# Kernel tuning notes

Measured on AMD Instinct MI355X. Metric: run time of the kernel, lower is better.

Reference implementation:

```python
import jax, jax.numpy as jnp
import numpy as np

STRIDES = [8, 16, 32, 64, 128]
FEAT_SIZES = [(100, 100), (50, 50), (25, 25), (13, 13), (7, 7)]
IMG_H, IMG_W = 800, 800
NUM_CLASSES = 8  # required by the repeat(8) in _loss_single_scale
BATCH, NUM_GT = 8, 50


def _make_anchor_levels():
    """RetinaNet anchors: octave_base_scale=4, scales_per_octave=3, ratios [0.5,1,2]."""
    ratios = np.array([0.5, 1.0, 2.0], dtype=np.float64)
    scales = 4.0 * 2.0 ** (np.arange(3) / 3.0)
    levels = []
    for stride, (fh, fw) in zip(STRIDES, FEAT_SIZES):
        h_r = np.sqrt(ratios)
        w_r = 1.0 / h_r
        ws = (w_r[:, None] * scales[None, :]).reshape(-1) * stride  # [9]
        hs = (h_r[:, None] * scales[None, :]).reshape(-1) * stride
        base = np.stack([-ws / 2, -hs / 2, ws / 2, hs / 2], axis=1)  # [9,4]
        xs = np.arange(fw) * stride
        ys = np.arange(fh) * stride
        xx, yy = np.meshgrid(xs, ys)  # [fh,fw]
        shifts = np.stack([xx, yy, xx, yy], axis=-1).reshape(-1, 4)  # [fh*fw,4]
        anchors = (shifts[:, None, :] + base[None, :, :]).reshape(-1, 4)  # loc-major, A inner
        levels.append(anchors.astype(np.float32))
    return levels


def _pairwise_iou(a, b):
    # a: [K,4], b: [G,4] -> [K,G]
    area_a = (a[:, 2] - a[:, 0]) * (a[:, 3] - a[:, 1])
    area_b = (b[:, 2] - b[:, 0]) * (b[:, 3] - b[:, 1])
    lt = jnp.maximum(a[:, None, :2], b[None, :, :2])
    rb = jnp.minimum(a[:, None, 2:], b[None, :, 2:])
    wh = jnp.clip(rb - lt, 0.0)
    inter = wh[..., 0] * wh[..., 1]
    return inter / (area_a[:, None] + area_b[None, :] - inter)


def _encode(anchors, gts):
    # DeltaXYWH encode, means=0, stds=1
    aw = anchors[:, 2] - anchors[:, 0]
    ah = anchors[:, 3] - anchors[:, 1]
    ax = anchors[:, 0] + 0.5 * aw
    ay = anchors[:, 1] + 0.5 * ah
    gw = gts[:, 2] - gts[:, 0]
    gh = gts[:, 3] - gts[:, 1]
    gx = gts[:, 0] + 0.5 * gw
    gy = gts[:, 1] + 0.5 * gh
    return jnp.stack([(gx - ax) / aw, (gy - ay) / ah,
                      jnp.log(gw / aw), jnp.log(gh / ah)], axis=1)


def _targets_per_image(anchors, tgt_boxes, tgt_cls):
    # MaxIoUMatcher(thresholds=[0.4,0.5], labels=[0,-1,1], low_quality=True)
    inside = ((anchors[:, 0] >= 0) & (anchors[:, 1] >= 0)
              & (anchors[:, 2] <= IMG_W) & (anchors[:, 3] <= IMG_H))
    iou = _pairwise_iou(anchors, tgt_boxes)             # [K,G]
    iou = jnp.where(inside[:, None], iou, -1.0)          # exclude outside anchors
    max_iou = iou.max(axis=1)
    argmax_gt = iou.argmax(axis=1)
    label = jnp.where(max_iou >= 0.5, 1, jnp.where(max_iou >= 0.4, -1, 0))
    gt_max = iou.max(axis=0)                             # [G]
    is_lq = (iou == gt_max[None, :]) & (gt_max[None, :] > 0)
    any_lq = is_lq.any(axis=1)
    G = tgt_boxes.shape[0]
    lq_gt = jnp.where(is_lq, jnp.arange(G)[None, :], -1).max(axis=1)
    matched_gt = jnp.where(any_lq, lq_gt, argmax_gt)
    label = jnp.where(any_lq, 1, label)
    pos = (label == 1) & inside
    neg = (label == 0) & inside
    deltas = _encode(anchors, tgt_boxes[matched_gt])     # [K,4]
    bbox_targets = jnp.where(pos[:, None], deltas, 0.0)
    bbox_weights = jnp.where(pos[:, None], 1.0, 0.0) * jnp.ones((1, 4), jnp.float32)
    labels_out = jnp.where(pos, tgt_cls[matched_gt].astype(jnp.float32), 0.0)
    label_weights = (pos | neg).astype(jnp.float32)
    return labels_out, label_weights, bbox_targets, bbox_weights, pos.sum(), neg.sum()


def _bce_logits(x, t):
    return jnp.maximum(x, 0.0) - x * t + jnp.log1p(jnp.exp(-jnp.abs(x)))


def _loss_level(cls_out, reg_out, labels, lw, bt, bw, num_samples):
    labels = labels.reshape(-1)
    lw = lw.reshape(-1)
    C = NUM_CLASSES
    cls_score = cls_out.transpose(0, 2, 3, 1).reshape(labels.shape[0], C)  # [N*H*W*A, C]
    tgt = jax.nn.one_hot(labels.astype(jnp.int32), C + 1, dtype=jnp.float32)[:, :C]
    lw2 = jnp.tile(lw, 8).reshape(-1, C)  # faithful to label_weights.repeat(8).reshape(-1, C)
    loss_cls = (_bce_logits(cls_score, tgt) * lw2).sum() / num_samples
    bt = bt.reshape(-1, 4)
    bw = bw.reshape(-1, 4)
    pred = reg_out.transpose(0, 2, 3, 1).reshape(-1, 4)
    loss_bbox = (jnp.abs(pred - bt) * bw).sum() / num_samples
    return loss_cls, loss_bbox


def setup_inputs() -> dict:
    key = jax.random.key(0)
    ks = jax.random.split(key, 16)
    inp = {}
    for i, (fh, fw) in enumerate(FEAT_SIZES):
        inp[f"cls{i}"] = jax.random.normal(ks[i], (BATCH, 9 * NUM_CLASSES, fh, fw), jnp.float32)
        inp[f"reg{i}"] = jax.random.normal(ks[5 + i], (BATCH, 9 * 4, fh, fw), jnp.float32)
    xy = jax.random.uniform(ks[10], (BATCH, NUM_GT, 2), minval=0.0, maxval=600.0)
    wh = jax.random.uniform(ks[11], (BATCH, NUM_GT, 2), minval=20.0, maxval=180.0)
    inp["target_boxes"] = jnp.concatenate([xy, xy + wh], axis=-1).astype(jnp.float32)
    inp["target_class_ids"] = jax.random.randint(ks[12], (BATCH, NUM_GT), 0, NUM_CLASSES, jnp.int64 if jax.config.jax_enable_x64 else jnp.int32)
    return inp


def reference(cls0, cls1, cls2, cls3, cls4, reg0, reg1, reg2, reg3, reg4,
              target_boxes, target_class_ids):
    anchor_levels = _make_anchor_levels()
    anchors = jnp.asarray(np.concatenate(anchor_levels, axis=0))  # [K,4]
    num_lvl = [a.shape[0] for a in anchor_levels]
    labels, lw, bt, bw, npos, nneg = jax.vmap(
        lambda b, c: _targets_per_image(anchors, b, c))(target_boxes, target_class_ids)
    num_samples = (npos.sum() + nneg.sum()).astype(jnp.float32)
    offs = np.cumsum([0] + num_lvl)
    cls_outs = [cls0, cls1, cls2, cls3, cls4]
    reg_outs = [reg0, reg1, reg2, reg3, reg4]
    loss_cls_all = jnp.float32(0.0)
    loss_bbox_all = jnp.float32(0.0)
    for i in range(len(num_lvl)):
        s, e = int(offs[i]), int(offs[i + 1])
        lc, lb = _loss_level(cls_outs[i], reg_outs[i], labels[:, s:e], lw[:, s:e],
                             bt[:, s:e], bw[:, s:e], num_samples)
        loss_cls_all = loss_cls_all + lc
        loss_bbox_all = loss_bbox_all + lb
    return loss_cls_all, loss_bbox_all
```

## Files before the change

kernel.cpp:

```cpp
#include <hip/hip_runtime.h>
#include <cstdint>

#define DEVINL __device__ __forceinline__

constexpr int NB = 8;
constexpr int NG = 50;
constexpr int KTOT = 120087;
constexpr int BK = NB * KTOT;

constexpr int L_W[5]   = {100, 50, 25, 13, 7};
constexpr int L_K[5]   = {90000, 22500, 5625, 1521, 441};
constexpr int L_OFF[5] = {0, 90000, 112500, 118125, 119646};
constexpr int L_STR[5] = {8, 16, 32, 64, 128};
constexpr int L_WSB[5] = {0, 720000, 900000, 945000, 957168};

constexpr double HR_T[3] = {0.7071067811865476, 1.0, 1.4142135623730951};
constexpr double WR_T[3] = {1.0 / HR_T[0], 1.0, 1.0 / HR_T[2]};
constexpr double SC_T[3] = {4.0, 5.039684199579493, 6.3496042078727974};

__device__ float4 g_anc[KTOT];
__device__ double g_accs[256][2];
__device__ unsigned g_ns;
__device__ unsigned g_gtmax[NB * NG];
__device__ int8_t g_lab[BK];
__device__ __align__(8) int8_t g_lw[BK];
__device__ int8_t g_pos[BK];
__device__ int8_t g_mg[BK];

DEVINL unsigned encf(float f) {
  unsigned u = __float_as_uint(f);
  return (u & 0x80000000u) ? ~u : (u | 0x80000000u);
}

DEVINL int lvl_of(int k) {
  return (k < 90000) ? 0 : (k < 112500) ? 1 : (k < 118125) ? 2 : (k < 119646) ? 3 : 4;
}

DEVINL float iou_one(float ax0, float ay0, float ax1, float ay1, float areaA,
                     float bx0, float by0, float bx1, float by1, float areaB) {
  float ltx = fmaxf(ax0, bx0);
  float lty = fmaxf(ay0, by0);
  float rbx = fminf(ax1, bx1);
  float rby = fminf(ay1, by1);
  float wx = fmaxf(rbx - ltx, 0.0f);
  float wy = fmaxf(rby - lty, 0.0f);
  float inter = wx * wy;
  return __fdividef(inter, areaA + areaB - inter);
}

__global__ __launch_bounds__(256) void k_setup() {
  if (blockIdx.x == 0) {
    int t = threadIdx.x;
    g_accs[t][0] = 0.0;
    g_accs[t][1] = 0.0;
    if (t == 0) g_ns = 0u;
  }
  int k = blockIdx.x * 256 + threadIdx.x;
  if (k >= KTOT) return;
  int l = lvl_of(k);
  int r = k - L_OFF[l];
  int loc = r / 9;
  int a = r - loc * 9;
  int W = L_W[l];
  int y = loc / W;
  int x = loc - y * W;
  int st = L_STR[l];
  int ridx = a / 3;
  int sidx = a - ridx * 3;
  double wsz = WR_T[ridx] * SC_T[sidx] * (double)st;
  double hsz = HR_T[ridx] * SC_T[sidx] * (double)st;
  double cx = (double)(x * st);
  double cy = (double)(y * st);
  g_anc[k] = make_float4((float)(cx - wsz * 0.5), (float)(cy - hsz * 0.5),
                         (float)(cx + wsz * 0.5), (float)(cy + hsz * 0.5));
}

DEVINL int axis_cand(int xi, int i0, int lo, int hi, int Wm1) {
  int c;
  if (xi < 4) c = i0 - 1 + xi;
  else if (xi == 4) c = lo;
  else if (xi == 5) c = lo + 1;
  else if (xi == 6) c = hi - 1;
  else if (xi == 7) c = hi;
  else if (xi == 8) c = 0;
  else c = Wm1;
  return min(max(c, 0), Wm1);
}

__global__ __launch_bounds__(256) void k_gtmax2(const float* __restrict__ tb) {
  const int bg = blockIdx.x;
  float4 v = reinterpret_cast<const float4*>(tb)[bg];
  const float bx0 = v.x, by0 = v.y, bx1 = v.z, by1 = v.w;
  const float areaB = (bx1 - bx0) * (by1 - by0);
  const float bcx = 0.5f * (bx0 + bx1), bcy = 0.5f * (by0 + by1);

  float m = -1.0f;
  for (int t = threadIdx.x; t < 4500; t += 256) {
    int l = t / 900;
    int rem = t - l * 900;
    int a = rem / 100;
    int rem2 = rem - a * 100;
    int xi = rem2 / 10;
    int yi = rem2 - xi * 10;
    int W = (l == 0) ? 100 : (l == 1) ? 50 : (l == 2) ? 25 : (l == 3) ? 13 : 7;
    int loff = (l == 0) ? 0 : (l == 1) ? 90000 : (l == 2) ? 112500
               : (l == 3) ? 118125 : 119646;
    float stf = (float)(8 << l);
    float4 A0 = g_anc[loff + a];
    float whalf = -A0.x;
    float hhalf = -A0.y;
    int i0x = (int)floorf(bcx / stf);
    int lox = (int)ceilf(whalf / stf);
    int hix = (int)floorf((800.0f - whalf) / stf);
    int i0y = (int)floorf(bcy / stf);
    int loy = (int)ceilf(hhalf / stf);
    int hiy = (int)floorf((800.0f - hhalf) / stf);
    int cx = axis_cand(xi, i0x, lox, hix, W - 1);
    int cy = axis_cand(yi, i0y, loy, hiy, W - 1);
    int k = loff + (cy * W + cx) * 9 + a;
    float4 A = g_anc[k];
    bool inside = (A.x >= 0.0f) & (A.y >= 0.0f) & (A.z <= 800.0f) & (A.w <= 800.0f);
    float areaA = (A.z - A.x) * (A.w - A.y);
    float iou = inside ? iou_one(A.x, A.y, A.z, A.w, areaA,
                                 bx0, by0, bx1, by1, areaB)
                       : -1.0f;
    m = fmaxf(m, iou);
  }
#pragma unroll
  for (int off = 32; off; off >>= 1) m = fmaxf(m, __shfl_down(m, off));
  __shared__ float s_m[4];
  int lane = threadIdx.x & 63, wid = threadIdx.x >> 6;
  if (lane == 0) s_m[wid] = m;
  __syncthreads();
  if (threadIdx.x == 0) {
    float r = fmaxf(fmaxf(s_m[0], s_m[1]), fmaxf(s_m[2], s_m[3]));
    g_gtmax[bg] = encf(r);
  }
}

constexpr int APB = 4;
__global__ __launch_bounds__(256) void k_assign(const float* __restrict__ tb,
                                                const int* __restrict__ tcls) {
  const int b = blockIdx.y;
  __shared__ float s_b[NG][8];
  __shared__ int s_cls[NG];
  __shared__ unsigned s_cnt;
  int tid = threadIdx.x;
  if (tid == 0) s_cnt = 0u;
  if (tid < NG) {
    float4 v = reinterpret_cast<const float4*>(tb)[b * NG + tid];
    s_b[tid][0] = v.x; s_b[tid][1] = v.y; s_b[tid][2] = v.z; s_b[tid][3] = v.w;
    s_b[tid][4] = (v.z - v.x) * (v.w - v.y);
    unsigned gm = g_gtmax[b * NG + tid];
    s_b[tid][5] = (gm > 0x80000000u) ? __uint_as_float(gm ^ 0x80000000u)
                                     : __uint_as_float(0x7FC00000u);
    s_cls[tid] = tcls[b * NG + tid];
  }
  __syncthreads();

  const int base = blockIdx.x * (256 * APB) + tid;
  float Ax0[APB], Ay0[APB], Ax1[APB], Ay1[APB], areaA[APB];
  bool inside[APB];
  float best[APB];
  int arg[APB], lqg[APB];
#pragma unroll
  for (int ap = 0; ap < APB; ++ap) {
    int k = base + ap * 256;
    bool valid = k < KTOT;
    float4 A = g_anc[valid ? k : 0];
    Ax0[ap] = A.x; Ay0[ap] = A.y; Ax1[ap] = A.z; Ay1[ap] = A.w;
    inside[ap] = valid & (A.x >= 0.0f) & (A.y >= 0.0f) & (A.z <= 800.0f) & (A.w <= 800.0f);
    areaA[ap] = (A.z - A.x) * (A.w - A.y);
    best[ap] = -2.0f; arg[ap] = 0; lqg[ap] = -1;
  }

#pragma unroll 5
  for (int g = 0; g < NG; ++g) {
    float gx0 = s_b[g][0], gy0 = s_b[g][1], gx1 = s_b[g][2], gy1 = s_b[g][3];
    float gar = s_b[g][4], qmx = s_b[g][5];
#pragma unroll
    for (int ap = 0; ap < APB; ++ap) {
      float iou = inside[ap] ? iou_one(Ax0[ap], Ay0[ap], Ax1[ap], Ay1[ap], areaA[ap],
                                       gx0, gy0, gx1, gy1, gar)
                             : -1.0f;
      if (iou > best[ap]) { best[ap] = iou; arg[ap] = g; }
      if (iou == qmx) lqg[ap] = g;
    }
  }

  int cnt = 0;
#pragma unroll
  for (int ap = 0; ap < APB; ++ap) {
    int k = base + ap * 256;
    if (k < KTOT) {
      int lab = (best[ap] >= 0.5f) ? 1 : ((best[ap] >= 0.4f) ? -1 : 0);
      int mg = arg[ap];
      if (lqg[ap] >= 0) { lab = 1; mg = lqg[ap]; }
      bool pos = (lab == 1) && inside[ap];
      bool neg = (lab == 0) && inside[ap];
      int l = lvl_of(k);
      int r = k - L_OFF[l];
      int widx = L_WSB[l] + b * L_K[l] + r;
      g_lab[widx] = pos ? (int8_t)s_cls[mg] : (int8_t)0;
      g_lw[widx] = (pos || neg) ? 1 : 0;
      g_pos[widx] = pos ? 1 : 0;
      g_mg[widx] = (int8_t)mg;
      cnt += (pos || neg) ? 1 : 0;
    }
  }
#pragma unroll
  for (int off = 32; off; off >>= 1) cnt += __shfl_down(cnt, off);
  if ((tid & 63) == 0 && cnt) atomicAdd(&s_cnt, (unsigned)cnt);
  __syncthreads();
  if (tid == 0 && s_cnt) atomicAdd(&g_ns, s_cnt);
}

template <int HW, int KL, int WSB, int LOFF>
DEVINL void level_term(const float* __restrict__ cls, const float* __restrict__ reg,
                       const float4* __restrict__ tb4, int j, bool valid,
                       float& vc, float& vb) {
  constexpr int NHW9 = 9 * HW;
  int b = j / NHW9;
  int r2 = j - b * NHW9;
  int a = r2 / HW;
  int pix = r2 - a * HW;
  int q = pix * 9 + a;
  int idx = WSB + b * KL + q;

  unsigned long long lwq =
      *reinterpret_cast<const unsigned long long*>(&g_lw[WSB + 8 * q]);
  int lab = g_lab[idx];
  const float* cbase = cls + (b * 72 + a * 8) * HW + pix;
  if (valid && lwq) {
#pragma unroll
    for (int c = 0; c < 8; ++c) {
      float w = (float)((unsigned)(lwq >> (8 * c)) & 0xffu);
      float x = cbase[c * HW];
      float t = (lab == c) ? 1.0f : 0.0f;
      float ax = fabsf(x);
      float e = __expf(-ax);
      float bce = fmaxf(x, 0.0f) - x * t + __logf(1.0f + e);
      vc += bce * w;
    }
  }
  int posb = valid ? g_pos[idx] : 0;
  if (posb) {
    int mg = g_mg[idx];
    float4 A = g_anc[LOFF + q];
    float aw = A.z - A.x, ah = A.w - A.y;
    float acx = A.x + 0.5f * aw, acy = A.y + 0.5f * ah;
    float4 gb = tb4[b * NG + mg];
    float gw = gb.z - gb.x, gh = gb.w - gb.y;
    float gcx = gb.x + 0.5f * gw, gcy = gb.y + 0.5f * gh;
    const float* rbase = reg + (b * 36 + a * 4) * HW + pix;
    vb += fabsf(rbase[0] - (gcx - acx) / aw);
    vb += fabsf(rbase[HW] - (gcy - acy) / ah);
    vb += fabsf(rbase[2 * HW] - logf(gw / aw));
    vb += fabsf(rbase[3 * HW] - logf(gh / ah));
  }
}

__global__ __launch_bounds__(256) void k_loss(
    const float* __restrict__ c0, const float* __restrict__ c1,
    const float* __restrict__ c2, const float* __restrict__ c3,
    const float* __restrict__ c4, const float* __restrict__ r0,
    const float* __restrict__ r1, const float* __restrict__ r2,
    const float* __restrict__ r3, const float* __restrict__ r4,
    const float* __restrict__ tb) {
  const float4* tb4 = reinterpret_cast<const float4*>(tb);
  int T = blockIdx.x * 256 + threadIdx.x;
  bool valid = T < BK;
  int Tc = valid ? T : 0;
  float vc = 0.0f, vb = 0.0f;
  if (Tc < 720000)       level_term<10000, 90000, 0, 0>(c0, r0, tb4, Tc, valid, vc, vb);
  else if (Tc < 900000)  level_term<2500, 22500, 720000, 90000>(c1, r1, tb4, Tc - 720000, valid, vc, vb);
  else if (Tc < 945000)  level_term<625, 5625, 900000, 112500>(c2, r2, tb4, Tc - 900000, valid, vc, vb);
  else if (Tc < 957168)  level_term<169, 1521, 945000, 118125>(c3, r3, tb4, Tc - 945000, valid, vc, vb);
  else                   level_term<49, 441, 957168, 119646>(c4, r4, tb4, Tc - 957168, valid, vc, vb);

#pragma unroll
  for (int off = 32; off; off >>= 1) {
    vc += __shfl_down(vc, off);
    vb += __shfl_down(vb, off);
  }
  __shared__ float sc_[4], sb_[4];
  int lane = threadIdx.x & 63;
  int wid = threadIdx.x >> 6;
  if (lane == 0) { sc_[wid] = vc; sb_[wid] = vb; }
  __syncthreads();
  if (threadIdx.x == 0) {
    float tc = sc_[0] + sc_[1] + sc_[2] + sc_[3];
    float tbx = sb_[0] + sb_[1] + sb_[2] + sb_[3];
    int slot = blockIdx.x & 255;
    if (tc != 0.0f) atomicAdd(&g_accs[slot][0], (double)tc);
    if (tbx != 0.0f) atomicAdd(&g_accs[slot][1], (double)tbx);
  }
}

__global__ __launch_bounds__(256) void k_fin(float* __restrict__ out) {
  int t = threadIdx.x;
  double a0 = g_accs[t][0];
  double a1 = g_accs[t][1];
#pragma unroll
  for (int off = 32; off; off >>= 1) {
    a0 += __shfl_down(a0, off);
    a1 += __shfl_down(a1, off);
  }
  __shared__ double s0[4], s1[4];
  if ((t & 63) == 0) { s0[t >> 6] = a0; s1[t >> 6] = a1; }
  __syncthreads();
  if (t == 0) {
    double A0 = s0[0] + s0[1] + s0[2] + s0[3];
    double A1 = s1[0] + s1[1] + s1[2] + s1[3];
    double n = (double)g_ns;
    out[0] = (float)(A0 / n);
    out[1] = (float)(A1 / n);
  }
}

extern "C" void kernel_launch(void* const* d_in, const int* in_sizes, int n_in,
                              void* d_out, int out_size, void* d_ws, size_t ws_size,
                              hipStream_t stream) {
  const float* c0 = (const float*)d_in[0];
  const float* r0 = (const float*)d_in[1];
  const float* c1 = (const float*)d_in[2];
  const float* r1 = (const float*)d_in[3];
  const float* c2 = (const float*)d_in[4];
  const float* r2 = (const float*)d_in[5];
  const float* c3 = (const float*)d_in[6];
  const float* r3 = (const float*)d_in[7];
  const float* c4 = (const float*)d_in[8];
  const float* r4 = (const float*)d_in[9];
  const float* tb = (const float*)d_in[10];
  const int* tcls = (const int*)d_in[11];
  float* out = (float*)d_out;

  k_setup<<<dim3((KTOT + 255) / 256), dim3(256), 0, stream>>>();
  k_gtmax2<<<dim3(NB * NG), dim3(256), 0, stream>>>(tb);
  k_assign<<<dim3((KTOT + 256 * APB - 1) / (256 * APB), NB), dim3(256), 0, stream>>>(tb, tcls);
  k_loss<<<dim3((BK + 255) / 256), dim3(256), 0, stream>>>(c0, c1, c2, c3, c4, r0, r1, r2,
                                                           r3, r4, tb);
  k_fin<<<dim3(1), dim3(256), 0, stream>>>(out);
}
```

Before: 166.2 us.

## Cull non-overlapping GT boxes per wavefront using anchor bounding extent

Each thread now handles contiguous anchors instead of anchors strided by the block width. Each wavefront reduces the union bounding box of its inside anchors with xor shuffles. A GT box's IoU loop is then skipped entirely when that box does not overlap the wavefront's extent. Outside anchors are moved to far-away dummy coordinates instead of being masked per IoU. This removes most IoU arithmetic for small-anchor levels. The cost is less coalesced loads and stores from the contiguous-per-thread indexing, and possible edge-case differences when a GT's max IoU is zero.

Result: faster. 157.3 us (-5.3%).

```diff
diff --git a/kernel.cpp b/kernel.cpp
--- a/kernel.cpp
+++ b/kernel.cpp
@@ -158,40 +158,59 @@
   }
   __syncthreads();
 
-  const int base = blockIdx.x * (256 * APB) + tid;
+  const int base = (blockIdx.x * 256 + tid) * APB;
   float Ax0[APB], Ay0[APB], Ax1[APB], Ay1[APB], areaA[APB];
   bool inside[APB];
+  float ex0 = __builtin_inff(), ey0 = __builtin_inff();
+  float ex1 = -__builtin_inff(), ey1 = -__builtin_inff();
+#pragma unroll
+  for (int ap = 0; ap < APB; ++ap) {
+    int k = base + ap;
+    bool valid = k < KTOT;
+    float4 A = g_anc[valid ? k : 0];
+    bool ins = valid & (A.x >= 0.0f) & (A.y >= 0.0f) & (A.z <= 800.0f) & (A.w <= 800.0f);
+    inside[ap] = ins;
+    ex0 = fminf(ex0, ins ? A.x : __builtin_inff());
+    ey0 = fminf(ey0, ins ? A.y : __builtin_inff());
+    ex1 = fmaxf(ex1, ins ? A.z : -__builtin_inff());
+    ey1 = fmaxf(ey1, ins ? A.w : -__builtin_inff());
+    if (!ins) A = make_float4(-4000.0f, -4000.0f, -3999.0f, -3999.0f);
+    Ax0[ap] = A.x; Ay0[ap] = A.y; Ax1[ap] = A.z; Ay1[ap] = A.w;
+    areaA[ap] = (A.z - A.x) * (A.w - A.y);
+  }
+#pragma unroll
+  for (int off = 1; off < 64; off <<= 1) {
+    ex0 = fminf(ex0, __shfl_xor(ex0, off));
+    ey0 = fminf(ey0, __shfl_xor(ey0, off));
+    ex1 = fmaxf(ex1, __shfl_xor(ex1, off));
+    ey1 = fmaxf(ey1, __shfl_xor(ey1, off));
+  }
+
   float best[APB];
   int arg[APB], lqg[APB];
 #pragma unroll
-  for (int ap = 0; ap < APB; ++ap) {
-    int k = base + ap * 256;
-    bool valid = k < KTOT;
-    float4 A = g_anc[valid ? k : 0];
-    Ax0[ap] = A.x; Ay0[ap] = A.y; Ax1[ap] = A.z; Ay1[ap] = A.w;
-    inside[ap] = valid & (A.x >= 0.0f) & (A.y >= 0.0f) & (A.z <= 800.0f) & (A.w <= 800.0f);
-    areaA[ap] = (A.z - A.x) * (A.w - A.y);
-    best[ap] = -2.0f; arg[ap] = 0; lqg[ap] = -1;
-  }
-
-#pragma unroll 5
+  for (int ap = 0; ap < APB; ++ap) { best[ap] = -2.0f; arg[ap] = 0; lqg[ap] = -1; }
+
   for (int g = 0; g < NG; ++g) {
     float gx0 = s_b[g][0], gy0 = s_b[g][1], gx1 = s_b[g][2], gy1 = s_b[g][3];
-    float gar = s_b[g][4], qmx = s_b[g][5];
-#pragma unroll
-    for (int ap = 0; ap < APB; ++ap) {
-      float iou = inside[ap] ? iou_one(Ax0[ap], Ay0[ap], Ax1[ap], Ay1[ap], areaA[ap],
-                                       gx0, gy0, gx1, gy1, gar)
-                             : -1.0f;
-      if (iou > best[ap]) { best[ap] = iou; arg[ap] = g; }
-      if (iou == qmx) lqg[ap] = g;
+    float ox = fminf(ex1, gx1) - fmaxf(ex0, gx0);
+    float oy = fminf(ey1, gy1) - fmaxf(ey0, gy0);
+    if (ox > 0.0f && oy > 0.0f) {
+      float gar = s_b[g][4], qmx = s_b[g][5];
+#pragma unroll
+      for (int ap = 0; ap < APB; ++ap) {
+        float iou = iou_one(Ax0[ap], Ay0[ap], Ax1[ap], Ay1[ap], areaA[ap],
+                            gx0, gy0, gx1, gy1, gar);
+        if (iou > best[ap]) { best[ap] = iou; arg[ap] = g; }
+        if (iou == qmx) lqg[ap] = g;
+      }
     }
   }
 
   int cnt = 0;
 #pragma unroll
   for (int ap = 0; ap < APB; ++ap) {
-    int k = base + ap * 256;
+    int k = base + ap;
     if (k < KTOT) {
       int lab = (best[ap] >= 0.5f) ? 1 : ((best[ap] >= 0.4f) ? -1 : 0);
       int mg = arg[ap];
```
